# Optimization experiments

Hardware: AMD Instinct MI355X
Metric: run time of the kernel (lower is better)

The kernel has to match this reference:

```python
import jax, jax.numpy as jnp
import numpy as np

WINDOW = 2048
STRIDE = 512
FREQ = WINDOW // 2  # 1024
FRAMES = 63
SIG_LEN = FRAMES * STRIDE  # 32256
BATCH = 64


def _make_kernels():
    # Hann window, sym=False: w[n] = 0.5*(1 - cos(2*pi*n/N))
    n = np.arange(WINDOW)
    window = 0.5 * (1.0 - np.cos(2.0 * np.pi * n / WINDOW))
    f = np.arange(FREQ)
    # basis[f, n] = exp(-2j*pi*f*n/N) * window[n]  (first N/2 rows of windowed DFT)
    phase = -2.0 * np.pi * np.outer(f, n) / WINDOW
    real = (np.cos(phase) * window[None, :]).T[:, None, :]  # [W, 1, F]
    imag = (np.sin(phase) * window[None, :]).T[:, None, :]  # [W, 1, F]
    return jnp.asarray(real, jnp.float32), jnp.asarray(imag, jnp.float32)


def setup_inputs() -> dict:
    key = jax.random.key(0)
    input_signal = jax.random.normal(key, (BATCH, SIG_LEN, 1), dtype=jnp.float32)
    real_kernel, imag_kernel = _make_kernels()
    return {"input_signal": input_signal, "real_kernel": real_kernel, "imag_kernel": imag_kernel}


def _stft(x, k):
    # TF 'same' padding for stride 512, kernel 2048, out = ceil(L/512) = 63:
    # total_pad = (out-1)*stride + kernel - L = 62*512 + 2048 - 32256 = 1536
    pad_l, pad_r = 768, 768
    return jax.lax.conv_general_dilated(
        x, k, window_strides=(STRIDE,), padding=[(pad_l, pad_r)],
        dimension_numbers=("NWC", "WIO", "NWC"))  # [B, 63, 1024]


def reference(input_signal, real_kernel, imag_kernel):
    real = _stft(input_signal, real_kernel)
    imag = _stft(input_signal, imag_kernel)
    real = real.reshape(-1, FRAMES, FREQ, 1)
    imag = imag.reshape(-1, FRAMES, FREQ, 1)
    return real, imag
```

## Files before the change

kernel.cpp:

```cpp
#include <hip/hip_runtime.h>
#include <hip/hip_bf16.h>
#include <math.h>

#define WINDOW   2048
#define STRIDE   512
#define FREQ     1024
#define FRAMES   63
#define SIG_LEN  32256
#define BATCH    64
#define M_TOTAL  4032
#define KD       1024

#define BM 128
#define BN 128
#define BK 64

#define UV_BLOCKS    2016
#define BASIS_BLOCKS 1024

typedef __attribute__((ext_vector_type(8)))  short short8;
typedef __attribute__((ext_vector_type(16))) float floatx16;

__device__ __forceinline__ ushort f2bf(float f) {
    __hip_bfloat16 h = __float2bfloat16(f);
    return *reinterpret_cast<ushort*>(&h);
}

__global__ __launch_bounds__(256) void prep_fused(
    const float* __restrict__ x, ushort* __restrict__ U,
    ushort* __restrict__ V, ushort* __restrict__ bt) {
    const int tid = threadIdx.x;
    if (blockIdx.x < UV_BLOCKS) {
        int id = blockIdx.x * 256 + tid;
        int r  = id >> 7;
        int n0 = (id & 127) * 8;
        int b  = r / FRAMES, t = r - b * FRAMES;
        int p0 = t * STRIDE + n0 - 768;
        int p1 = p0 + 1024;
        float x0[8] = {0,0,0,0,0,0,0,0}, x1[8] = {0,0,0,0,0,0,0,0};
        const float* xb = x + (size_t)b * SIG_LEN;
        if (p0 >= 0 && p0 + 8 <= SIG_LEN) {
            float4 a = *(const float4*)(xb + p0), c = *(const float4*)(xb + p0 + 4);
            x0[0]=a.x; x0[1]=a.y; x0[2]=a.z; x0[3]=a.w;
            x0[4]=c.x; x0[5]=c.y; x0[6]=c.z; x0[7]=c.w;
        }
        if (p1 >= 0 && p1 + 8 <= SIG_LEN) {
            float4 a = *(const float4*)(xb + p1), c = *(const float4*)(xb + p1 + 4);
            x1[0]=a.x; x1[1]=a.y; x1[2]=a.z; x1[3]=a.w;
            x1[4]=c.x; x1[5]=c.y; x1[6]=c.z; x1[7]=c.w;
        }
        ushort uo[8], vo[8];
        const float c0 = 6.28318530717958648f / 2048.f;
#pragma unroll
        for (int j = 0; j < 8; ++j) {
            int n = n0 + j;
            float w0 = 0.5f - 0.5f * __cosf(c0 * (float)n);
            float w1 = 0.5f - 0.5f * __cosf(c0 * (float)(n + 1024));
            float a = x0[j] * w0, bb = x1[j] * w1;
            uo[j] = f2bf(a + bb);
            vo[j] = f2bf(a - bb);
        }
        *(uint4*)(U + (size_t)r * KD + n0) = *(uint4*)uo;
        *(uint4*)(V + (size_t)r * KD + n0) = *(uint4*)vo;
    } else {
        int id = (blockIdx.x - UV_BLOCKS) * 256 + tid;
        int c  = id >> 7;
        int n0 = (id & 127) * 8;
        int cls = c >> 9, g = c & 511;
        int f = 2 * g + (cls & 1);
        ushort o[8];
        const float step = 6.28318530717958648f / 2048.f;
#pragma unroll
        for (int j = 0; j < 8; ++j) {
            int m = (f * (n0 + j)) & 2047;
            float th = step * (float)m;
            float val = (cls < 2) ? __cosf(th) : -__sinf(th);
            o[j] = f2bf(val);
        }
        *(uint4*)(bt + (size_t)c * KD + n0) = *(uint4*)o;
    }
}

__device__ __forceinline__ void gload16(const ushort* g, ushort* l) {
    __builtin_amdgcn_global_load_lds(
        (const __attribute__((address_space(1))) unsigned int*)g,
        (__attribute__((address_space(3))) unsigned int*)l,
        16, 0, 0);
}

__global__ __launch_bounds__(256) void stft_gemm(
    const ushort* __restrict__ U, const ushort* __restrict__ V,
    const ushort* __restrict__ bt, float* __restrict__ out) {
    __shared__ __align__(16) ushort As[2 * BM * 32];
    __shared__ __align__(16) ushort Bs[2 * BN * 32];

    const int tid  = threadIdx.x;
    const int lane = tid & 63;
    const int w    = tid >> 6;
    const int mtile = blockIdx.x;
    const int ntile = blockIdx.y;
    const int cls   = ntile & 3;
    const int ctile = ntile >> 2;

    const int srow = w * 16 + (lane >> 2);
    const int kcol = ((lane & 3) ^ ((lane >> 3) & 3)) * 8;

    const ushort* Apt = (cls & 1) ? V : U;
    int gr0 = mtile * BM + srow;
    int gr1 = gr0 + 64;
    gr0 = min(gr0, M_TOTAL - 1);
    gr1 = min(gr1, M_TOTAL - 1);
    const ushort* gA0 = Apt + (size_t)gr0 * KD + kcol;
    const ushort* gA1 = Apt + (size_t)gr1 * KD + kcol;
    const ushort* gB0 = bt + (size_t)(cls * 512 + ctile * BN + srow) * KD + kcol;
    const ushort* gB1 = gB0 + (size_t)64 * KD;

    ushort* ldsA0 = As + w * 512;
    ushort* ldsA1 = As + 2048 + w * 512;
    ushort* ldsB0 = Bs + w * 512;
    ushort* ldsB1 = Bs + 2048 + w * 512;

    const int wm = w >> 1, wn = w & 1;
    const int fr32 = lane & 31;
    const int kg   = lane >> 5;
    const int rsw  = (fr32 >> 1) & 3;
    const ushort* pA = As + (wm * 64 + fr32) * 32;
    const ushort* pB = Bs + (wn * 64 + fr32) * 32;

    floatx16 acc[2][2];
#pragma unroll
    for (int mi = 0; mi < 2; ++mi)
#pragma unroll
        for (int ni = 0; ni < 2; ++ni)
#pragma unroll
            for (int r = 0; r < 16; ++r) acc[mi][ni][r] = 0.f;

    for (int kt = 0; kt < KD / BK; ++kt) {
        __syncthreads();
        gload16(gA0,      ldsA0);
        gload16(gA0 + 32, ldsA0 + 4096);
        gload16(gA1,      ldsA1);
        gload16(gA1 + 32, ldsA1 + 4096);
        gload16(gB0,      ldsB0);
        gload16(gB0 + 32, ldsB0 + 4096);
        gload16(gB1,      ldsB1);
        gload16(gB1 + 32, ldsB1 + 4096);
        gA0 += BK; gA1 += BK; gB0 += BK; gB1 += BK;
        __syncthreads();

#pragma unroll
        for (int s = 0; s < 4; ++s) {
            const int off = (s >> 1) * 4096 + (((s & 1) * 2 + kg) ^ rsw) * 8;
            short8 a[2], b[2];
#pragma unroll
            for (int mi = 0; mi < 2; ++mi)
                a[mi] = *(const short8*)(pA + mi * 32 * 32 + off);
#pragma unroll
            for (int ni = 0; ni < 2; ++ni)
                b[ni] = *(const short8*)(pB + ni * 32 * 32 + off);
#pragma unroll
            for (int mi = 0; mi < 2; ++mi)
#pragma unroll
                for (int ni = 0; ni < 2; ++ni)
                    acc[mi][ni] = __builtin_amdgcn_mfma_f32_32x32x16_bf16(
                        a[mi], b[ni], acc[mi][ni], 0, 0, 0);
        }
    }

    const int orow_base = mtile * BM + wm * 64;
    float* outp = out + (size_t)(cls >> 1) * M_TOTAL * FREQ;
    const int fbase = 2 * (ctile * BN + wn * 64 + fr32) + (cls & 1);

#pragma unroll
    for (int mi = 0; mi < 2; ++mi) {
#pragma unroll
        for (int r = 0; r < 16; ++r) {
            int grow = orow_base + mi * 32 + (r & 3) + 8 * (r >> 2) + 4 * kg;
            if (grow < M_TOTAL) {
                float* orow = outp + (size_t)grow * FREQ + fbase;
#pragma unroll
                for (int ni = 0; ni < 2; ++ni)
                    orow[ni * 64] = acc[mi][ni][r];
            }
        }
    }
}

extern "C" void kernel_launch(void* const* d_in, const int* in_sizes, int n_in,
                              void* d_out, int out_size, void* d_ws, size_t ws_size,
                              hipStream_t stream) {
    const float* x = (const float*)d_in[0];

    ushort* U   = (ushort*)d_ws;
    ushort* V   = U + (size_t)M_TOTAL * KD;
    ushort* btm = V + (size_t)M_TOTAL * KD;

    prep_fused<<<UV_BLOCKS + BASIS_BLOCKS, 256, 0, stream>>>(x, U, V, btm);
    stft_gemm<<<dim3((M_TOTAL + BM - 1) / BM, 16), 256, 0, stream>>>(
        U, V, btm, (float*)d_out);
}
```

Measured before the change: 106.7 us.

## Double-buffer LDS staging in STFT GEMM and share window cosine

The GEMM main loop now prefetches the next K-tile into a second LDS buffer via global_load_lds while computing on the current one. Explicit vmcnt waits and barriers replace the two __syncthreads per iteration, and s_setprio raises wave priority around the MFMA block. The prep kernel reuses one cosine for both Hann window halves, using cos(x+pi) = -cos(x). LDS use doubles to 64KB per block, which may cut occupancy, and the hand-written waitcnt counts must match the eight loads issued per stage.

```diff
diff --git a/kernel.cpp b/kernel.cpp
--- a/kernel.cpp
+++ b/kernel.cpp
@@ -54,8 +54,9 @@
 #pragma unroll
         for (int j = 0; j < 8; ++j) {
             int n = n0 + j;
-            float w0 = 0.5f - 0.5f * __cosf(c0 * (float)n);
-            float w1 = 0.5f - 0.5f * __cosf(c0 * (float)(n + 1024));
+            float cn = __cosf(c0 * (float)n);
+            float w0 = 0.5f - 0.5f * cn;
+            float w1 = 0.5f + 0.5f * cn;
             float a = x0[j] * w0, bb = x1[j] * w1;
             uo[j] = f2bf(a + bb);
             vo[j] = f2bf(a - bb);
@@ -91,8 +92,8 @@
 __global__ __launch_bounds__(256) void stft_gemm(
     const ushort* __restrict__ U, const ushort* __restrict__ V,
     const ushort* __restrict__ bt, float* __restrict__ out) {
-    __shared__ __align__(16) ushort As[2 * BM * 32];
-    __shared__ __align__(16) ushort Bs[2 * BN * 32];
+    __shared__ __align__(16) ushort As[2 * 8192];
+    __shared__ __align__(16) ushort Bs[2 * 8192];
 
     const int tid  = threadIdx.x;
     const int lane = tid & 63;
@@ -115,11 +116,6 @@
     const ushort* gB0 = bt + (size_t)(cls * 512 + ctile * BN + srow) * KD + kcol;
     const ushort* gB1 = gB0 + (size_t)64 * KD;
 
-    ushort* ldsA0 = As + w * 512;
-    ushort* ldsA1 = As + 2048 + w * 512;
-    ushort* ldsB0 = Bs + w * 512;
-    ushort* ldsB1 = Bs + 2048 + w * 512;
-
     const int wm = w >> 1, wn = w & 1;
     const int fr32 = lane & 31;
     const int kg   = lane >> 5;
@@ -135,22 +131,25 @@
 #pragma unroll
             for (int r = 0; r < 16; ++r) acc[mi][ni][r] = 0.f;
 
-    for (int kt = 0; kt < KD / BK; ++kt) {
-        __syncthreads();
-        gload16(gA0,      ldsA0);
-        gload16(gA0 + 32, ldsA0 + 4096);
-        gload16(gA1,      ldsA1);
-        gload16(gA1 + 32, ldsA1 + 4096);
-        gload16(gB0,      ldsB0);
-        gload16(gB0 + 32, ldsB0 + 4096);
-        gload16(gB1,      ldsB1);
-        gload16(gB1 + 32, ldsB1 + 4096);
+    auto STAGE = [&](int buf) {
+        ushort* Ab = As + buf * 8192 + w * 512;
+        ushort* Bb = Bs + buf * 8192 + w * 512;
+        gload16(gA0,      Ab);
+        gload16(gA0 + 32, Ab + 4096);
+        gload16(gA1,      Ab + 2048);
+        gload16(gA1 + 32, Ab + 6144);
+        gload16(gB0,      Bb);
+        gload16(gB0 + 32, Bb + 4096);
+        gload16(gB1,      Bb + 2048);
+        gload16(gB1 + 32, Bb + 6144);
         gA0 += BK; gA1 += BK; gB0 += BK; gB1 += BK;
-        __syncthreads();
-
+    };
+
+    auto COMPUTE = [&](int buf) {
+        const int bo = buf * 8192;
 #pragma unroll
         for (int s = 0; s < 4; ++s) {
-            const int off = (s >> 1) * 4096 + (((s & 1) * 2 + kg) ^ rsw) * 8;
+            const int off = bo + (s >> 1) * 4096 + (((s & 1) * 2 + kg) ^ rsw) * 8;
             short8 a[2], b[2];
 #pragma unroll
             for (int mi = 0; mi < 2; ++mi)
@@ -158,14 +157,36 @@
 #pragma unroll
             for (int ni = 0; ni < 2; ++ni)
                 b[ni] = *(const short8*)(pB + ni * 32 * 32 + off);
+            __builtin_amdgcn_s_setprio(1);
 #pragma unroll
             for (int mi = 0; mi < 2; ++mi)
 #pragma unroll
                 for (int ni = 0; ni < 2; ++ni)
                     acc[mi][ni] = __builtin_amdgcn_mfma_f32_32x32x16_bf16(
                         a[mi], b[ni], acc[mi][ni], 0, 0, 0);
-        }
+            __builtin_amdgcn_s_setprio(0);
+        }
+    };
+
+    STAGE(0);
+    for (int kt = 0; kt < KD / BK - 1; ++kt) {
+        const int cur = kt & 1;
+        STAGE(cur ^ 1);
+        asm volatile("s_waitcnt vmcnt(8)" ::: "memory");
+        __builtin_amdgcn_sched_barrier(0);
+        __builtin_amdgcn_s_barrier();
+        __builtin_amdgcn_sched_barrier(0);
+        COMPUTE(cur);
+        asm volatile("s_waitcnt lgkmcnt(0)" ::: "memory");
+        __builtin_amdgcn_sched_barrier(0);
+        __builtin_amdgcn_s_barrier();
+        __builtin_amdgcn_sched_barrier(0);
     }
+    asm volatile("s_waitcnt vmcnt(0)" ::: "memory");
+    __builtin_amdgcn_sched_barrier(0);
+    __builtin_amdgcn_s_barrier();
+    __builtin_amdgcn_sched_barrier(0);
+    COMPUTE(1);
 
     const int orow_base = mtile * BM + wm * 64;
     float* outp = out + (size_t)(cls >> 1) * M_TOTAL * FREQ;
```

After: 108.6 us. No clear change (+1.8%).
